# Kernel tuning notes

Hardware: AMD Instinct MI355X
Metric: run time of the kernel (lower is better)

The kernel has to match this reference:

```python
import jax, jax.numpy as jnp
import numpy as np

B, TQ, TK, D = 16, 1024, 4096, 512


def setup_inputs() -> dict:
    key = jax.random.key(0)
    k1, k2, k3 = jax.random.split(key, 3)
    decoder_output = jax.random.normal(k1, (B, TQ, D), dtype=jnp.float32)
    encoder_output = jax.random.normal(k2, (B, TK, D), dtype=jnp.float32)
    # Keras Dense(lstm_size): kernel [D, D] (glorot-ish scale), bias [D] (zeros init)
    W_a = jax.random.normal(k3, (D, D), dtype=jnp.float32) * (1.0 / np.sqrt(D))
    b_a = jnp.zeros((D,), dtype=jnp.float32)
    return {"decoder_output": decoder_output, "encoder_output": encoder_output,
            "W_a": W_a, "b_a": b_a}


def reference(decoder_output, encoder_output, W_a, b_a):
    # Luong 'general' attention:
    # proj = Dense(encoder_output)            [B, Tk, D]
    proj = jnp.einsum('bkd,de->bke', encoder_output, W_a) + b_a
    # score = dec @ proj^T                    [B, Tq, Tk]
    score = jnp.einsum('bqd,bkd->bqk', decoder_output, proj)
    # softmax over encoder time axis (tf axis=2 == last axis here)
    alignment_vector = jax.nn.softmax(score, axis=-1)
    # context = align @ encoder_output        [B, Tq, D]
    context_vector = jnp.einsum('bqk,bkd->bqd', alignment_vector, encoder_output)
    return (context_vector, alignment_vector)
```

## Files before the change

### kernel.cpp

```cpp
#include <hip/hip_runtime.h>
#include <hip/hip_bf16.h>

#define B_  16
#define TQ_ 1024
#define TK_ 4096
#define D_  512

typedef unsigned short u16;
typedef __attribute__((ext_vector_type(8))) short short8;
typedef __attribute__((ext_vector_type(8))) _Float16 f16x8;
typedef __attribute__((ext_vector_type(4))) float f32x4;

__device__ __forceinline__ u16 bf16_rne(float x) {
  unsigned u = __float_as_uint(x);
  u += 0x7FFFu + ((u >> 16) & 1u);
  return (u16)(u >> 16);
}
__device__ __forceinline__ float bf16_as_f32(u16 h) {
  return __uint_as_float(((unsigned)h) << 16);
}
__device__ __forceinline__ void split_bf16(float x, u16& h, u16& l) {
  u16 hh = bf16_rne(x);
  h = hh;
  l = bf16_rne(x - bf16_as_f32(hh));
}

__device__ __forceinline__ void glld16(const void* g, void* lds) {
  __builtin_amdgcn_global_load_lds(
      (const __attribute__((address_space(1))) unsigned int*)g,
      (__attribute__((address_space(3))) unsigned int*)lds, 16, 0, 0);
}

__device__ __forceinline__ int seg_src4(int l) {
  return (l & 3) ^ ((l >> 2) & 3) ^ ((l >> 4) & 3);
}

__global__ __launch_bounds__(256) void split_planes_kernel(
    const float* __restrict__ X, u16* __restrict__ H, u16* __restrict__ L,
    int n8)
{
  int i = blockIdx.x * 256 + threadIdx.x;
  if (i >= n8) return;
  const float4* src = (const float4*)X + (size_t)i * 2;
  float4 a = src[0], b = src[1];
  __align__(16) u16 h[8], l[8];
  split_bf16(a.x, h[0], l[0]);
  split_bf16(a.y, h[1], l[1]);
  split_bf16(a.z, h[2], l[2]);
  split_bf16(a.w, h[3], l[3]);
  split_bf16(b.x, h[4], l[4]);
  split_bf16(b.y, h[5], l[5]);
  split_bf16(b.z, h[6], l[6]);
  split_bf16(b.w, h[7], l[7]);
  *(uint4*)&H[(size_t)i * 8] = *(const uint4*)h;
  *(uint4*)&L[(size_t)i * 8] = *(const uint4*)l;
}

__global__ __launch_bounds__(256) void transpose_conv_kernel(
    const float* __restrict__ E, _Float16* __restrict__ ET,
    _Float16* __restrict__ EF)
{
  __shared__ float tile[64][65];
  const int b  = blockIdx.z;
  const int k0 = blockIdx.x * 64;
  const int d0 = blockIdx.y * 64;
  const float* Eb = E + (long long)b * TK_ * D_;
  _Float16* ETb = ET + (long long)b * D_ * TK_;

  const int t  = threadIdx.x;
  const int r  = t >> 2;
  const int c4 = (t & 3) * 16;

  __align__(16) _Float16 g[16];
  #pragma unroll
  for (int i = 0; i < 16; i += 4) {
    float4 v = *(const float4*)&Eb[(long long)(k0 + r) * D_ + d0 + c4 + i];
    tile[r][c4 + i + 0] = v.x;
    tile[r][c4 + i + 1] = v.y;
    tile[r][c4 + i + 2] = v.z;
    tile[r][c4 + i + 3] = v.w;
    g[i + 0] = (_Float16)v.x;
    g[i + 1] = (_Float16)v.y;
    g[i + 2] = (_Float16)v.z;
    g[i + 3] = (_Float16)v.w;
  }
  if (EF) {
    _Float16* EFb = EF + (long long)b * TK_ * D_;
    uint4* dstF = (uint4*)&EFb[(long long)(k0 + r) * D_ + d0 + c4];
    dstF[0] = ((const uint4*)g)[0];
    dstF[1] = ((const uint4*)g)[1];
  }
  __syncthreads();

  __align__(16) _Float16 h[16];
  #pragma unroll
  for (int i = 0; i < 16; ++i) h[i] = (_Float16)tile[c4 + i][r];
  uint4* dst = (uint4*)&ETb[(long long)(d0 + r) * TK_ + k0 + c4];
  dst[0] = ((const uint4*)h)[0];
  dst[1] = ((const uint4*)h)[1];
}

#define D2BM 64
#define D2BN 128
#define D2BK 32
#define D2NT (D_ / D2BK)

__global__ __launch_bounds__(256) void gemm_dec2p_kernel(
    const u16* __restrict__ Ahp, const u16* __restrict__ Alp,
    const u16* __restrict__ Bhp, const u16* __restrict__ Blp,
    _Float16* __restrict__ Ch, _Float16* __restrict__ Cl)
{
  __shared__ u16 sAh[2][D2BM * D2BK];
  __shared__ u16 sAl[2][D2BM * D2BK];
  __shared__ u16 sBh[2][D2BN * D2BK];
  __shared__ u16 sBl[2][D2BN * D2BK];

  const int m0 = blockIdx.y * D2BM;
  const int n0 = blockIdx.x * D2BN;

  const int t    = threadIdx.x;
  const int lane = t & 63;
  const int wave = t >> 6;
  const int wrm  = (wave >> 1) * 32;
  const int wcn  = (wave & 1) * 64;
  const int ln   = lane & 15;
  const int qd   = lane >> 4;
  const int sw   = qd ^ (ln & 3) ^ (ln >> 2);

  f32x4 acc[2][4];
  #pragma unroll
  for (int i = 0; i < 2; ++i)
    #pragma unroll
    for (int j = 0; j < 4; ++j) { f32x4 z = {0.f,0.f,0.f,0.f}; acc[i][j] = z; }

  const int ab = seg_src4(lane) * 16;
  const char* gAh = (const char*)Ahp + (long long)(m0 + wave * 16 + (lane >> 2)) * D_ * 2 + ab;
  const char* gAl = (const char*)Alp + (long long)(m0 + wave * 16 + (lane >> 2)) * D_ * 2 + ab;
  const int adst = wave * 1024 + lane * 16;
  const char* gBh = (const char*)Bhp + (long long)(n0 + wave * 32 + (lane >> 2)) * D_ * 2 + ab;
  const char* gBl = (const char*)Blp + (long long)(n0 + wave * 32 + (lane >> 2)) * D_ * 2 + ab;
  const long long rstep = (long long)16 * D_ * 2;
  const int bdst = wave * 2048 + lane * 16;

  auto stage = [&](int buf, int k0) {
    const long long ko = (long long)k0 * 2;
    glld16(gAh + ko, (char*)sAh[buf] + adst);
    glld16(gAl + ko, (char*)sAl[buf] + adst);
    glld16(gBh + ko, (char*)sBh[buf] + bdst);
    glld16(gBh + ko + rstep, (char*)sBh[buf] + bdst + 1024);
    glld16(gBl + ko, (char*)sBl[buf] + bdst);
    glld16(gBl + ko + rstep, (char*)sBl[buf] + bdst + 1024);
  };

  stage(0, 0);
  __syncthreads();

  #pragma unroll
  for (int tt = 0; tt < D2NT; ++tt) {
    const int cur = tt & 1;
    if (tt + 1 < D2NT) stage(cur ^ 1, (tt + 1) * D2BK);
    __builtin_amdgcn_sched_barrier(0);

    short8 fah[2], fal[2], fbh[4], fbl[4];
    #pragma unroll
    for (int i = 0; i < 2; ++i) {
      const int ra = (wrm + i * 16 + ln) * D2BK + sw * 8;
      fah[i] = *(const short8*)&sAh[cur][ra];
      fal[i] = *(const short8*)&sAl[cur][ra];
    }
    #pragma unroll
    for (int j = 0; j < 4; ++j) {
      const int rb = (wcn + j * 16 + ln) * D2BK + sw * 8;
      fbh[j] = *(const short8*)&sBh[cur][rb];
      fbl[j] = *(const short8*)&sBl[cur][rb];
    }
    __builtin_amdgcn_s_setprio(1);
    #pragma unroll
    for (int i = 0; i < 2; ++i)
      #pragma unroll
      for (int j = 0; j < 4; ++j) {
        acc[i][j] = __builtin_amdgcn_mfma_f32_16x16x32_bf16(fah[i], fbh[j], acc[i][j], 0, 0, 0);
        acc[i][j] = __builtin_amdgcn_mfma_f32_16x16x32_bf16(fah[i], fbl[j], acc[i][j], 0, 0, 0);
        acc[i][j] = __builtin_amdgcn_mfma_f32_16x16x32_bf16(fal[i], fbh[j], acc[i][j], 0, 0, 0);
      }
    __builtin_amdgcn_s_setprio(0);
    __syncthreads();
  }

  #pragma unroll
  for (int i = 0; i < 2; ++i)
    #pragma unroll
    for (int j = 0; j < 4; ++j)
      #pragma unroll
      for (int rg = 0; rg < 4; ++rg) {
        int row = m0 + wrm + i * 16 + qd * 4 + rg;
        int col = n0 + wcn + j * 16 + ln;
        float x = acc[i][j][rg];
        _Float16 h = (_Float16)x;
        _Float16 l = (_Float16)(x - (float)h);
        long long idx = (long long)row * D_ + col;
        Ch[idx] = h;
        Cl[idx] = l;
      }
}

#define DBM 128
#define DBN 128
#define DBK 32
#define DPAD 40

__global__ __launch_bounds__(256) void gemm_dec2_kernel(
    const float* __restrict__ A, const float* __restrict__ Bm,
    _Float16* __restrict__ Ch, _Float16* __restrict__ Cl)
{
  __shared__ u16 Ah[DBM * DPAD];
  __shared__ u16 Al[DBM * DPAD];
  __shared__ u16 Bh[DBN * DPAD];
  __shared__ u16 Bl[DBN * DPAD];

  const float* Ab = A  + (long long)(blockIdx.y * DBM) * D_;
  const float* Bb = Bm + (long long)(blockIdx.x * DBN) * D_;

  const int t    = threadIdx.x;
  const int r    = t >> 1;
  const int hf   = t & 1;
  const int lane = t & 63;
  const int wave = t >> 6;
  const int wr   = (wave >> 1) * 64;
  const int wc   = (wave & 1) * 64;
  const int ln   = lane & 15;
  const int qd   = lane >> 4;

  f32x4 acc[4][4];
  #pragma unroll
  for (int i = 0; i < 4; ++i)
    #pragma unroll
    for (int j = 0; j < 4; ++j) { f32x4 z = {0.f,0.f,0.f,0.f}; acc[i][j] = z; }

  const float* srcA = Ab + (long long)r * D_ + hf * 16;
  const float* srcB = Bb + (long long)r * D_ + hf * 16;
  u16* dAh = &Ah[r * DPAD + hf * 16];
  u16* dAl = &Al[r * DPAD + hf * 16];
  u16* dBh = &Bh[r * DPAD + hf * 16];
  u16* dBl = &Bl[r * DPAD + hf * 16];

  for (int k0 = 0; k0 < D_; k0 += DBK) {
    {
      __align__(16) u16 h[16], l[16];
      #pragma unroll
      for (int i = 0; i < 16; i += 4) {
        float4 v = *(const float4*)(srcA + k0 + i);
        split_bf16(v.x, h[i+0], l[i+0]);
        split_bf16(v.y, h[i+1], l[i+1]);
        split_bf16(v.z, h[i+2], l[i+2]);
        split_bf16(v.w, h[i+3], l[i+3]);
      }
      ((uint4*)dAh)[0] = ((const uint4*)h)[0];
      ((uint4*)dAh)[1] = ((const uint4*)h)[1];
      ((uint4*)dAl)[0] = ((const uint4*)l)[0];
      ((uint4*)dAl)[1] = ((const uint4*)l)[1];
      #pragma unroll
      for (int i = 0; i < 16; i += 4) {
        float4 v = *(const float4*)(srcB + k0 + i);
        split_bf16(v.x, h[i+0], l[i+0]);
        split_bf16(v.y, h[i+1], l[i+1]);
        split_bf16(v.z, h[i+2], l[i+2]);
        split_bf16(v.w, h[i+3], l[i+3]);
      }
      ((uint4*)dBh)[0] = ((const uint4*)h)[0];
      ((uint4*)dBh)[1] = ((const uint4*)h)[1];
      ((uint4*)dBl)[0] = ((const uint4*)l)[0];
      ((uint4*)dBl)[1] = ((const uint4*)l)[1];
    }
    __syncthreads();

    short8 fah[4], fal[4], fbh[4], fbl[4];
    #pragma unroll
    for (int i = 0; i < 4; ++i) {
      int ra = (wr + i * 16 + ln) * DPAD + qd * 8;
      int rb = (wc + i * 16 + ln) * DPAD + qd * 8;
      fah[i] = *(const short8*)&Ah[ra];
      fal[i] = *(const short8*)&Al[ra];
      fbh[i] = *(const short8*)&Bh[rb];
      fbl[i] = *(const short8*)&Bl[rb];
    }
    #pragma unroll
    for (int i = 0; i < 4; ++i)
      #pragma unroll
      for (int j = 0; j < 4; ++j) {
        acc[i][j] = __builtin_amdgcn_mfma_f32_16x16x32_bf16(fah[i], fbh[j], acc[i][j], 0, 0, 0);
        acc[i][j] = __builtin_amdgcn_mfma_f32_16x16x32_bf16(fah[i], fbl[j], acc[i][j], 0, 0, 0);
        acc[i][j] = __builtin_amdgcn_mfma_f32_16x16x32_bf16(fal[i], fbh[j], acc[i][j], 0, 0, 0);
      }
    __syncthreads();
  }

  const int m0 = blockIdx.y * DBM;
  const int n0 = blockIdx.x * DBN;
  #pragma unroll
  for (int i = 0; i < 4; ++i)
    #pragma unroll
    for (int j = 0; j < 4; ++j)
      #pragma unroll
      for (int rg = 0; rg < 4; ++rg) {
        int row = m0 + wr + i * 16 + qd * 4 + rg;
        int col = n0 + wc + j * 16 + ln;
        float x = acc[i][j][rg];
        _Float16 h = (_Float16)x;
        _Float16 l = (_Float16)(x - (float)h);
        long long idx = (long long)row * D_ + col;
        Ch[idx] = h;
        Cl[idx] = l;
      }
}

#define SBM 128
#define SBN 128
#define SBK 32
#define S_NT (D_ / SBK)

template<bool F16B>
__global__ __launch_bounds__(256) void gemm_score_kernel(
    const _Float16* __restrict__ A_h, const _Float16* __restrict__ A_l,
    const float* __restrict__ Bf, const _Float16* __restrict__ B16,
    float* __restrict__ C)
{
  __shared__ _Float16 sAh[2][SBM * SBK];
  __shared__ _Float16 sAl[2][SBM * SBK];
  __shared__ _Float16 sB [2][SBN * SBK];

  const int bz = blockIdx.z;
  const int m0 = blockIdx.y * SBM;
  const int n0 = blockIdx.x * SBN;
  const _Float16* Ahb = A_h + (long long)bz * TQ_ * D_ + (long long)m0 * D_;
  const _Float16* Alb = A_l + (long long)bz * TQ_ * D_ + (long long)m0 * D_;

  const int t    = threadIdx.x;
  const int lane = t & 63;
  const int wave = t >> 6;
  const int wr   = (wave >> 1) * 64;
  const int wc   = (wave & 1) * 64;
  const int ln   = lane & 15;
  const int qd   = lane >> 4;
  const int sw   = qd ^ (ln & 3) ^ (ln >> 2);

  f32x4 acc[4][4];
  #pragma unroll
  for (int i = 0; i < 4; ++i)
    #pragma unroll
    for (int j = 0; j < 4; ++j) { f32x4 z = {0.f,0.f,0.f,0.f}; acc[i][j] = z; }

  const int c0   = wave * 2;
  const int arow = c0 * 16 + (lane >> 2);
  const int ab   = seg_src4(lane) * 16;
  const char* gAh = (const char*)Ahb + (long long)arow * D_ * 2 + ab;
  const char* gAl = (const char*)Alb + (long long)arow * D_ * 2 + ab;
  const long long rstep = (long long)16 * D_ * 2;
  const int dstoff = c0 * 1024 + lane * 16;

  const char* gB16 = nullptr;
  if constexpr (F16B) {
    const _Float16* Bb16 = B16 + (long long)bz * TK_ * D_ + (long long)n0 * D_;
    gB16 = (const char*)Bb16 + (long long)arow * D_ * 2 + ab;
  }

  const float* Bb = Bf + (long long)bz * TK_ * D_ + (long long)n0 * D_;
  const int brow = t >> 1;
  const int bhf  = t & 1;
  const float* srcB = Bb + (long long)brow * D_ + bhf * 16;
  const int bh2 = (brow & 3) ^ ((brow >> 2) & 3);
  const int db0 = brow * SBK + ((2 * bhf    ) ^ bh2) * 8;
  const int db1 = brow * SBK + ((2 * bhf + 1) ^ bh2) * 8;

  auto stage = [&](int buf, int k0) {
    const long long ko = (long long)k0 * 2;
    char* dAh = (char*)sAh[buf] + dstoff;
    char* dAl = (char*)sAl[buf] + dstoff;
    glld16(gAh + ko, dAh);
    glld16(gAh + ko + rstep, dAh + 1024);
    glld16(gAl + ko, dAl);
    glld16(gAl + ko + rstep, dAl + 1024);
    if constexpr (F16B) {
      char* dBv = (char*)sB[buf] + dstoff;
      glld16(gB16 + ko, dBv);
      glld16(gB16 + ko + rstep, dBv + 1024);
    } else {
      __align__(16) _Float16 hb[16];
      #pragma unroll
      for (int i = 0; i < 16; i += 4) {
        float4 v = *(const float4*)(srcB + k0 + i);
        hb[i+0] = (_Float16)v.x;
        hb[i+1] = (_Float16)v.y;
        hb[i+2] = (_Float16)v.z;
        hb[i+3] = (_Float16)v.w;
      }
      *(uint4*)&sB[buf][db0] = ((const uint4*)hb)[0];
      *(uint4*)&sB[buf][db1] = ((const uint4*)hb)[1];
    }
  };

  stage(0, 0);
  __syncthreads();

  #pragma unroll
  for (int tt = 0; tt < S_NT; ++tt) {
    const int cur = tt & 1;
    if (tt + 1 < S_NT) stage(cur ^ 1, (tt + 1) * SBK);
    __builtin_amdgcn_sched_barrier(0);

    f16x8 fah[4], fal[4], fb[4];
    #pragma unroll
    for (int i = 0; i < 4; ++i) {
      const int ra = (wr + i * 16 + ln) * SBK + sw * 8;
      const int rb = (wc + i * 16 + ln) * SBK + sw * 8;
      fah[i] = *(const f16x8*)&sAh[cur][ra];
      fal[i] = *(const f16x8*)&sAl[cur][ra];
      fb[i]  = *(const f16x8*)&sB[cur][rb];
    }
    __builtin_amdgcn_s_setprio(1);
    #pragma unroll
    for (int i = 0; i < 4; ++i)
      #pragma unroll
      for (int j = 0; j < 4; ++j) {
        acc[i][j] = __builtin_amdgcn_mfma_f32_16x16x32_f16(fah[i], fb[j], acc[i][j], 0, 0, 0);
        acc[i][j] = __builtin_amdgcn_mfma_f32_16x16x32_f16(fal[i], fb[j], acc[i][j], 0, 0, 0);
      }
    __builtin_amdgcn_s_setprio(0);
    __syncthreads();
  }

  float* Cb = C + (long long)bz * TQ_ * TK_;
  #pragma unroll
  for (int i = 0; i < 4; ++i)
    #pragma unroll
    for (int j = 0; j < 4; ++j)
      #pragma unroll
      for (int rg = 0; rg < 4; ++rg) {
        int row = m0 + wr + i * 16 + qd * 4 + rg;
        int col = n0 + wc + j * 16 + ln;
        Cb[(long long)row * TK_ + col] = acc[i][j][rg];
      }
}

template<bool WP16>
__global__ __launch_bounds__(256) void softmax_kernel(
    float* __restrict__ P, _Float16* __restrict__ P16)
{
  __shared__ float red[8];
  float* p = P + (long long)blockIdx.x * TK_;
  const int t    = threadIdx.x;
  const int lane = t & 63;
  const int wave = t >> 6;

  float4 v[4];
  float mx = -3.0e38f;
  #pragma unroll
  for (int i = 0; i < 4; ++i) {
    v[i] = *(const float4*)&p[i * 1024 + t * 4];
    mx = fmaxf(mx, fmaxf(fmaxf(v[i].x, v[i].y), fmaxf(v[i].z, v[i].w)));
  }
  #pragma unroll
  for (int o = 32; o > 0; o >>= 1) mx = fmaxf(mx, __shfl_xor(mx, o, 64));
  if (lane == 0) red[wave] = mx;
  __syncthreads();
  mx = fmaxf(fmaxf(red[0], red[1]), fmaxf(red[2], red[3]));

  float s = 0.f;
  #pragma unroll
  for (int i = 0; i < 4; ++i) {
    v[i].x = __expf(v[i].x - mx);
    v[i].y = __expf(v[i].y - mx);
    v[i].z = __expf(v[i].z - mx);
    v[i].w = __expf(v[i].w - mx);
    s += (v[i].x + v[i].y) + (v[i].z + v[i].w);
  }
  #pragma unroll
  for (int o = 32; o > 0; o >>= 1) s += __shfl_xor(s, o, 64);
  if (lane == 0) red[4 + wave] = s;
  __syncthreads();
  s = (red[4] + red[5]) + (red[6] + red[7]);
  const float inv = 1.0f / s;

  _Float16* p16 = WP16 ? (P16 + (long long)blockIdx.x * TK_) : nullptr;
  #pragma unroll
  for (int i = 0; i < 4; ++i) {
    v[i].x *= inv; v[i].y *= inv; v[i].z *= inv; v[i].w *= inv;
    *(float4*)&p[i * 1024 + t * 4] = v[i];
    if constexpr (WP16) {
      union { _Float16 h[4]; uint2 u; } pk;
      pk.h[0] = (_Float16)v[i].x;
      pk.h[1] = (_Float16)v[i].y;
      pk.h[2] = (_Float16)v[i].z;
      pk.h[3] = (_Float16)v[i].w;
      *(uint2*)&p16[i * 1024 + t * 4] = pk.u;
    }
  }
}

#define CBM 64
#define CBN 128
#define CBK 32
#define C_NT (TK_ / CBK)

template<bool F16A>
__global__ __launch_bounds__(256) void gemm_ctx_kernel(
    const float* __restrict__ P, const _Float16* __restrict__ P16,
    const _Float16* __restrict__ ET, float* __restrict__ C)
{
  __shared__ _Float16 sA[3][CBM * CBK];
  __shared__ _Float16 sB[3][CBN * CBK];

  const int bid = blockIdx.x;
  const int s   = (bid & 7) * 128 + (bid >> 3);
  const int m0  = (s & 15) * CBM;
  const int n0  = ((s >> 4) & 3) * CBN;
  const int bz  = s >> 6;

  const float*    Pb = P  + (long long)bz * TQ_ * TK_ + (long long)m0 * TK_;
  const _Float16* Eb = ET + (long long)bz * D_ * TK_  + (long long)n0 * TK_;

  const int t    = threadIdx.x;
  const int lane = t & 63;
  const int wave = t >> 6;
  const int wr   = (wave >> 1) * 32;
  const int wc   = (wave & 1) * 64;
  const int ln   = lane & 15;
  const int qd   = lane >> 4;
  const int sw   = qd ^ (ln & 3) ^ (ln >> 2);

  f32x4 acc[2][4];
  #pragma unroll
  for (int i = 0; i < 2; ++i)
    #pragma unroll
    for (int j = 0; j < 4; ++j) { f32x4 z = {0.f,0.f,0.f,0.f}; acc[i][j] = z; }

  const int ab = seg_src4(lane) * 16;
  const char* gB = (const char*)Eb + ((long long)(wave * 32 + (lane >> 2)) * TK_) * 2 + ab;
  const long long rstepB = (long long)16 * TK_ * 2;
  const int bdst = wave * 2048 + lane * 16;
  const char* gA16 = nullptr;
  if constexpr (F16A) {
    const _Float16* Pb16 = P16 + (long long)bz * TQ_ * TK_ + (long long)m0 * TK_;
    gA16 = (const char*)Pb16 + ((long long)(wave * 16 + (lane >> 2)) * TK_) * 2 + ab;
  }
  const int adst = wave * 1024 + lane * 16;

  const int arowf = t >> 2;
  const int asegf = t & 3;
  const float* gAf = Pb + (long long)arowf * TK_ + asegf * 8;
  const int afoff = arowf * CBK + ((asegf ^ (arowf & 3) ^ ((arowf >> 2) & 3)) * 8);

  auto stage = [&](int buf, int k0) {
    const long long ko = (long long)k0 * 2;
    char* dB = (char*)sB[buf] + bdst;
    glld16(gB + ko, dB);
    glld16(gB + ko + rstepB, dB + 1024);
    if constexpr (F16A) {
      glld16(gA16 + ko, (char*)sA[buf] + adst);
    } else {
      float4 v0 = *(const float4*)(gAf + k0);
      float4 v1 = *(const float4*)(gAf + k0 + 4);
      __align__(16) _Float16 hb[8];
      hb[0] = (_Float16)v0.x; hb[1] = (_Float16)v0.y;
      hb[2] = (_Float16)v0.z; hb[3] = (_Float16)v0.w;
      hb[4] = (_Float16)v1.x; hb[5] = (_Float16)v1.y;
      hb[6] = (_Float16)v1.z; hb[7] = (_Float16)v1.w;
      *(uint4*)&sA[buf][afoff] = *(const uint4*)hb;
    }
  };

  stage(0, 0);
  stage(1, CBK);
  if constexpr (F16A) {
    asm volatile("s_waitcnt vmcnt(3)" ::: "memory");
  } else {
    asm volatile("s_waitcnt vmcnt(0) lgkmcnt(0)" ::: "memory");
  }
  __builtin_amdgcn_s_barrier();
  __builtin_amdgcn_sched_barrier(0);

  int cur = 0, nxt = 2;
  #pragma unroll 1
  for (int tt = 0; tt < C_NT; ++tt) {
    if (tt + 2 < C_NT) stage(nxt, (tt + 2) * CBK);

    const _Float16* bA  = sA[cur];
    const _Float16* bBv = sB[cur];
    f16x8 fa[2], fb[4];
    #pragma unroll
    for (int i = 0; i < 2; ++i)
      fa[i] = *(const f16x8*)&bA[(wr + i * 16 + ln) * CBK + sw * 8];
    #pragma unroll
    for (int j = 0; j < 4; ++j)
      fb[j] = *(const f16x8*)&bBv[(wc + j * 16 + ln) * CBK + sw * 8];
    __builtin_amdgcn_s_setprio(1);
    #pragma unroll
    for (int i = 0; i < 2; ++i)
      #pragma unroll
      for (int j = 0; j < 4; ++j)
        acc[i][j] = __builtin_amdgcn_mfma_f32_16x16x32_f16(fa[i], fb[j], acc[i][j], 0, 0, 0);
    __builtin_amdgcn_s_setprio(0);
    if (tt + 1 < C_NT) {
      if constexpr (F16A) {
        if (tt + 2 < C_NT) {
          asm volatile("s_waitcnt vmcnt(3)" ::: "memory");
        } else {
          asm volatile("s_waitcnt vmcnt(0)" ::: "memory");
        }
      } else {
        asm volatile("s_waitcnt vmcnt(0) lgkmcnt(0)" ::: "memory");
      }
      __builtin_amdgcn_s_barrier();
      __builtin_amdgcn_sched_barrier(0);
    }
    cur = (cur == 2) ? 0 : cur + 1;
    nxt = (nxt == 2) ? 0 : nxt + 1;
  }

  float* Cb = C + (long long)bz * TQ_ * D_;
  #pragma unroll
  for (int i = 0; i < 2; ++i)
    #pragma unroll
    for (int j = 0; j < 4; ++j)
      #pragma unroll
      for (int rg = 0; rg < 4; ++rg) {
        int row = m0 + wr + i * 16 + qd * 4 + rg;
        int col = n0 + wc + j * 16 + ln;
        Cb[(long long)row * D_ + col] = acc[i][j][rg];
      }
}

extern "C" void kernel_launch(void* const* d_in, const int* in_sizes, int n_in,
                              void* d_out, int out_size, void* d_ws, size_t ws_size,
                              hipStream_t stream) {
  (void)in_sizes; (void)n_in; (void)out_size;
  const float* dec = (const float*)d_in[0];
  const float* enc = (const float*)d_in[1];
  const float* Wa  = (const float*)d_in[2];

  float* ctx   = (float*)d_out;
  float* align = ctx + (long long)B_ * TQ_ * D_;

  char* ws = (char*)d_ws;
  const size_t SZ_ENCT = (size_t)B_ * D_ * TK_ * 2;
  const size_t SZ_DEC2 = (size_t)B_ * TQ_ * D_ * 2;
  const size_t SZ_ENCF = (size_t)B_ * TK_ * D_ * 2;
  const size_t SZ_P16  = (size_t)B_ * TQ_ * TK_ * 2;
  const size_t SZ_WB   = (size_t)D_ * D_ * 2;

  _Float16* encT  = (_Float16*)(ws);
  _Float16* dec2h = (_Float16*)(ws + SZ_ENCT);
  _Float16* dec2l = (_Float16*)(ws + SZ_ENCT + SZ_DEC2);
  _Float16* encF  = (_Float16*)(ws + SZ_ENCT + 2 * SZ_DEC2);
  _Float16* p16   = (_Float16*)(ws + SZ_ENCT);
  u16* dech = (u16*)(ws + SZ_ENCT + SZ_P16);
  u16* decl = dech + (size_t)B_ * TQ_ * D_;
  u16* Wh   = decl + (size_t)B_ * TQ_ * D_;
  u16* Wl   = Wh + (size_t)D_ * D_;

  const bool mid  = ws_size >= SZ_ENCT + 2 * SZ_DEC2 + SZ_ENCF;
  const bool full = ws_size >= SZ_ENCT + SZ_P16;
  const bool pre  = ws_size >= SZ_ENCT + SZ_P16 + 2 * SZ_DEC2 + 2 * SZ_WB;

  transpose_conv_kernel<<<dim3(TK_ / 64, D_ / 64, B_), 256, 0, stream>>>(
      enc, encT, mid ? encF : nullptr);

  if (pre) {
    split_planes_kernel<<<dim3((B_ * TQ_ * D_ / 8) / 256), 256, 0, stream>>>(
        dec, dech, decl, B_ * TQ_ * D_ / 8);
    split_planes_kernel<<<dim3((D_ * D_ / 8) / 256), 256, 0, stream>>>(
        Wa, Wh, Wl, D_ * D_ / 8);
    gemm_dec2p_kernel<<<dim3(D_ / D2BN, (B_ * TQ_) / D2BM), 256, 0, stream>>>(
        dech, decl, Wh, Wl, dec2h, dec2l);
  } else {
    gemm_dec2_kernel<<<dim3(D_ / DBN, (B_ * TQ_) / DBM), 256, 0, stream>>>(
        dec, Wa, dec2h, dec2l);
  }

  if (mid)
    gemm_score_kernel<true><<<dim3(TK_ / SBN, TQ_ / SBM, B_), 256, 0, stream>>>(
        dec2h, dec2l, enc, encF, align);
  else
    gemm_score_kernel<false><<<dim3(TK_ / SBN, TQ_ / SBM, B_), 256, 0, stream>>>(
        dec2h, dec2l, enc, nullptr, align);

  if (full)
    softmax_kernel<true><<<B_ * TQ_, 256, 0, stream>>>(align, p16);
  else
    softmax_kernel<false><<<B_ * TQ_, 256, 0, stream>>>(align, nullptr);

  if (full)
    gemm_ctx_kernel<true><<<dim3((TQ_ / CBM) * (D_ / CBN) * B_), 256, 0, stream>>>(
        align, p16, encT, ctx);
  else
    gemm_ctx_kernel<false><<<dim3((TQ_ / CBM) * (D_ / CBN) * B_), 256, 0, stream>>>(
        align, nullptr, encT, ctx);
}
```

Before: 850.8 us.

## Halve score GEMM M-tile and use triple-buffered LDS with vmcnt waits

Shrinks the score GEMM block tile from 128x128 to 64x128, so each wave holds a 32x64 accumulator, and moves from double to triple LDS buffering that prefetches two K-steps ahead. Each block-wide __syncthreads is replaced by an explicit s_waitcnt vmcnt plus s_barrier, so loads already in flight for the next stage need not drain. The aim is more blocks in flight, better latency hiding and fewer stalls at barriers. In exchange each loaded B tile is reused across fewer rows, which raises global traffic per FLOP, and the hand-counted vmcnt values must match the number of outstanding loads exactly.

```diff
diff --git a/kernel.cpp b/kernel.cpp
--- a/kernel.cpp
+++ b/kernel.cpp
@@ -314,7 +314,7 @@
       }
 }
 
-#define SBM 128
+#define SBM 64
 #define SBN 128
 #define SBK 32
 #define S_NT (D_ / SBK)
@@ -325,9 +325,9 @@
     const float* __restrict__ Bf, const _Float16* __restrict__ B16,
     float* __restrict__ C)
 {
-  __shared__ _Float16 sAh[2][SBM * SBK];
-  __shared__ _Float16 sAl[2][SBM * SBK];
-  __shared__ _Float16 sB [2][SBN * SBK];
+  __shared__ _Float16 sAh[3][SBM * SBK];
+  __shared__ _Float16 sAl[3][SBM * SBK];
+  __shared__ _Float16 sB [3][SBN * SBK];
 
   const int bz = blockIdx.z;
   const int m0 = blockIdx.y * SBM;
@@ -338,30 +338,28 @@
   const int t    = threadIdx.x;
   const int lane = t & 63;
   const int wave = t >> 6;
-  const int wr   = (wave >> 1) * 64;
+  const int wr   = (wave >> 1) * 32;
   const int wc   = (wave & 1) * 64;
   const int ln   = lane & 15;
   const int qd   = lane >> 4;
   const int sw   = qd ^ (ln & 3) ^ (ln >> 2);
 
-  f32x4 acc[4][4];
-  #pragma unroll
-  for (int i = 0; i < 4; ++i)
+  f32x4 acc[2][4];
+  #pragma unroll
+  for (int i = 0; i < 2; ++i)
     #pragma unroll
     for (int j = 0; j < 4; ++j) { f32x4 z = {0.f,0.f,0.f,0.f}; acc[i][j] = z; }
 
-  const int c0   = wave * 2;
-  const int arow = c0 * 16 + (lane >> 2);
-  const int ab   = seg_src4(lane) * 16;
-  const char* gAh = (const char*)Ahb + (long long)arow * D_ * 2 + ab;
-  const char* gAl = (const char*)Alb + (long long)arow * D_ * 2 + ab;
+  const int ab = seg_src4(lane) * 16;
+  const char* gAh = (const char*)Ahb + (long long)(wave * 16 + (lane >> 2)) * D_ * 2 + ab;
+  const char* gAl = (const char*)Alb + (long long)(wave * 16 + (lane >> 2)) * D_ * 2 + ab;
+  const int adst = wave * 1024 + lane * 16;
   const long long rstep = (long long)16 * D_ * 2;
-  const int dstoff = c0 * 1024 + lane * 16;
-
+  const int bdst = wave * 2048 + lane * 16;
   const char* gB16 = nullptr;
   if constexpr (F16B) {
     const _Float16* Bb16 = B16 + (long long)bz * TK_ * D_ + (long long)n0 * D_;
-    gB16 = (const char*)Bb16 + (long long)arow * D_ * 2 + ab;
+    gB16 = (const char*)Bb16 + (long long)(wave * 32 + (lane >> 2)) * D_ * 2 + ab;
   }
 
   const float* Bb = Bf + (long long)bz * TK_ * D_ + (long long)n0 * D_;
@@ -374,14 +372,10 @@
 
   auto stage = [&](int buf, int k0) {
     const long long ko = (long long)k0 * 2;
-    char* dAh = (char*)sAh[buf] + dstoff;
-    char* dAl = (char*)sAl[buf] + dstoff;
-    glld16(gAh + ko, dAh);
-    glld16(gAh + ko + rstep, dAh + 1024);
-    glld16(gAl + ko, dAl);
-    glld16(gAl + ko + rstep, dAl + 1024);
+    glld16(gAh + ko, (char*)sAh[buf] + adst);
+    glld16(gAl + ko, (char*)sAl[buf] + adst);
     if constexpr (F16B) {
-      char* dBv = (char*)sB[buf] + dstoff;
+      char* dBv = (char*)sB[buf] + bdst;
       glld16(gB16 + ko, dBv);
       glld16(gB16 + ko + rstep, dBv + 1024);
     } else {
@@ -400,38 +394,58 @@
   };
 
   stage(0, 0);
-  __syncthreads();
+  stage(1, SBK);
+  if constexpr (F16B) {
+    asm volatile("s_waitcnt vmcnt(4)" ::: "memory");
+  } else {
+    asm volatile("s_waitcnt vmcnt(0) lgkmcnt(0)" ::: "memory");
+  }
+  __builtin_amdgcn_s_barrier();
+  __builtin_amdgcn_sched_barrier(0);
 
   #pragma unroll
   for (int tt = 0; tt < S_NT; ++tt) {
-    const int cur = tt & 1;
-    if (tt + 1 < S_NT) stage(cur ^ 1, (tt + 1) * SBK);
-    __builtin_amdgcn_sched_barrier(0);
-
-    f16x8 fah[4], fal[4], fb[4];
-    #pragma unroll
-    for (int i = 0; i < 4; ++i) {
+    const int cur = tt % 3;
+    const int nxt = (tt + 2) % 3;
+    if (tt + 2 < S_NT) stage(nxt, (tt + 2) * SBK);
+
+    f16x8 fah[2], fal[2], fb[4];
+    #pragma unroll
+    for (int i = 0; i < 2; ++i) {
       const int ra = (wr + i * 16 + ln) * SBK + sw * 8;
-      const int rb = (wc + i * 16 + ln) * SBK + sw * 8;
       fah[i] = *(const f16x8*)&sAh[cur][ra];
       fal[i] = *(const f16x8*)&sAl[cur][ra];
-      fb[i]  = *(const f16x8*)&sB[cur][rb];
-    }
+    }
+    #pragma unroll
+    for (int j = 0; j < 4; ++j)
+      fb[j] = *(const f16x8*)&sB[cur][(wc + j * 16 + ln) * SBK + sw * 8];
     __builtin_amdgcn_s_setprio(1);
     #pragma unroll
-    for (int i = 0; i < 4; ++i)
+    for (int i = 0; i < 2; ++i)
       #pragma unroll
       for (int j = 0; j < 4; ++j) {
         acc[i][j] = __builtin_amdgcn_mfma_f32_16x16x32_f16(fah[i], fb[j], acc[i][j], 0, 0, 0);
         acc[i][j] = __builtin_amdgcn_mfma_f32_16x16x32_f16(fal[i], fb[j], acc[i][j], 0, 0, 0);
       }
     __builtin_amdgcn_s_setprio(0);
-    __syncthreads();
+    if (tt + 1 < S_NT) {
+      if constexpr (F16B) {
+        if (tt + 2 < S_NT) {
+          asm volatile("s_waitcnt vmcnt(4)" ::: "memory");
+        } else {
+          asm volatile("s_waitcnt vmcnt(0)" ::: "memory");
+        }
+      } else {
+        asm volatile("s_waitcnt vmcnt(0) lgkmcnt(0)" ::: "memory");
+      }
+      __builtin_amdgcn_s_barrier();
+      __builtin_amdgcn_sched_barrier(0);
+    }
   }
 
   float* Cb = C + (long long)bz * TQ_ * TK_;
   #pragma unroll
-  for (int i = 0; i < 4; ++i)
+  for (int i = 0; i < 2; ++i)
     #pragma unroll
     for (int j = 0; j < 4; ++j)
       #pragma unroll
```

After: 874.0 us. +2.7%, slower.
